# Optimization experiments

Measured on AMD Instinct MI355X. Metric: run time of the kernel, lower is better.

The kernel has to match this reference:

```python
import jax, jax.numpy as jnp
import numpy as np

B, S, D = 2, 4096, 2048
H = 16
HD = D // H          # head dim = 128
CHUNK = 64           # chunk size for O(N) chunked linear attention


def setup_inputs() -> dict:
    key = jax.random.key(0)
    ks = jax.random.split(key, 5)
    w = D ** -0.5  # fan-in init scale
    return {
        "x": jax.random.normal(ks[0], (B, S, D), jnp.float32),
        "Wq": jax.random.normal(ks[1], (D, D), jnp.float32) * w,
        "Wk": jax.random.normal(ks[2], (D, D), jnp.float32) * w,
        "Wv": jax.random.normal(ks[3], (D, D), jnp.float32) * w,
        "Wo": jax.random.normal(ks[4], (D, D), jnp.float32) * w,
    }


def _chunk_linear_attn(q, k, v):
    """Causal linear attention (identity feature map), chunked recurrent form.
    q, k, v: [b, h, n, d]. Equivalent to o_t = sum_{s<=t} (q_t . k_s) v_s.
    """
    b, h, n, d = q.shape
    nc = n // CHUNK
    q = q.reshape(b, h, nc, CHUNK, d)
    k = k.reshape(b, h, nc, CHUNK, d)
    v = v.reshape(b, h, nc, CHUNK, d)
    # intra-chunk causal part
    attn = jnp.einsum('bhncd,bhnsd->bhncs', q, k)
    causal = jnp.tril(jnp.ones((CHUNK, CHUNK), dtype=bool))
    attn = jnp.where(causal, attn, jnp.zeros((), attn.dtype))
    o_intra = jnp.einsum('bhncs,bhnsd->bhncd', attn, v)
    # inter-chunk recurrent state: S_i = sum_{j < i} K_j^T V_j  ([d, d] per head)
    kv = jnp.einsum('bhnsd,bhnse->bhnde', k, v)
    S = jnp.cumsum(kv, axis=2) - kv  # exclusive prefix sum over chunks
    o_inter = jnp.einsum('bhncd,bhnde->bhnce', q, S)
    return (o_intra + o_inter).reshape(b, h, n, d)


def reference(x, Wq, Wk, Wv, Wo):
    # bias-free projections (nn.Linear convention: y = x @ W.T)
    q = (x @ Wq.T).reshape(B, S, H, HD).transpose(0, 2, 1, 3)
    k = (x @ Wk.T).reshape(B, S, H, HD).transpose(0, 2, 1, 3)
    v = (x @ Wv.T).reshape(B, S, H, HD).transpose(0, 2, 1, 3)
    scale = HD ** -0.5  # fla chunk_linear_attn default scale on q
    o = _chunk_linear_attn(q * scale, k, v)
    o = o.transpose(0, 2, 1, 3).reshape(B, S, D)
    return o @ Wo.T
```

## Files before the change

### kernel.cpp

```cpp
#include <hip/hip_runtime.h>

typedef unsigned short u16;
typedef __attribute__((ext_vector_type(8))) short short8;
typedef __attribute__((ext_vector_type(8))) unsigned short u16x8;
typedef __attribute__((ext_vector_type(4))) unsigned short u16x4;
typedef __attribute__((ext_vector_type(2))) unsigned short u16x2;
typedef __attribute__((ext_vector_type(4))) float f32x4;

#define NBATCH 2
#define SEQ    4096
#define DIM    2048
#define NHEAD  16
#define HD     128
#define CH     64
#define NC     64
#define MROWS  8192

__device__ __forceinline__ float b2f(u16 u) {
    unsigned x = ((unsigned)u) << 16;
    return __builtin_bit_cast(float, x);
}
__device__ __forceinline__ u16 f2b(float f) {
    unsigned u = __builtin_bit_cast(unsigned, f);
    u += 0x7fffu + ((u >> 16) & 1u);
    return (u16)(u >> 16);
}

__device__ __forceinline__ void gload_lds16(const u16* g, u16* l) {
    __builtin_amdgcn_global_load_lds(
        (const __attribute__((address_space(1))) void*)g,
        (__attribute__((address_space(3))) void*)l, 16, 0, 0);
}

__global__ __launch_bounds__(256) void cast_all(
    const float* __restrict__ x,
    const float* __restrict__ w0, const float* __restrict__ w1,
    const float* __restrict__ w2, const float* __restrict__ w3,
    u16* __restrict__ xo,
    u16* __restrict__ o0, u16* __restrict__ o1,
    u16* __restrict__ o2, u16* __restrict__ o3)
{
    const int blk = blockIdx.x;
    const float* in;
    u16* out;
    long i;
    if (blk < 8192) {
        in = x; out = xo;
        i = (long)blk * 256 + threadIdx.x;
    } else {
        const int seg = (blk - 8192) >> 11;
        in  = seg == 0 ? w0 : seg == 1 ? w1 : seg == 2 ? w2 : w3;
        out = seg == 0 ? o0 : seg == 1 ? o1 : seg == 2 ? o2 : o3;
        i = (long)((blk - 8192) & 2047) * 256 + threadIdx.x;
    }
    f32x4 a = ((const f32x4*)in)[2 * i];
    f32x4 b = ((const f32x4*)in)[2 * i + 1];
    u16x8 o;
#pragma unroll
    for (int j = 0; j < 4; j++) { o[j] = f2b(a[j]); o[4 + j] = f2b(b[j]); }
    ((u16x8*)out)[i] = o;
}

#define GBM 256
#define GBN 256
#define GBK 32
#define BUFE 16384

struct Ctx8 {
    int wave, lane, wr, wc, m16, quad;
    int fl;
    long grA[2];
    int ldso[2];
};

__device__ __forceinline__ Ctx8 ctx8(int K) {
    Ctx8 c;
    const int tid = threadIdx.x;
    c.wave = tid >> 6; c.lane = tid & 63;
    c.wr = c.wave >> 2; c.wc = c.wave & 3;
    c.m16 = c.lane & 15; c.quad = (c.lane >> 4) & 3;
    const int t3 = c.lane >> 3;
    const int u3 = (c.lane & 7) ^ t3;
    const int ml = 2 * t3 + (u3 >> 2);
    const int sl = (u3 & 3) * 8;
#pragma unroll
    for (int i = 0; i < 2; i++) {
        const int bi = 2 * c.wave + i;
        c.grA[i] = (long)(bi * 16 + ml) * K + sl;
        c.ldso[i] = bi * 512 + c.lane * 8;
    }
    const int line = c.m16 >> 1;
    c.fl = line * 64 + ((((c.m16 & 1) << 2) | c.quad) ^ line) * 8;
    return c;
}

template<bool STG>
__device__ __forceinline__ void tile8(
    const Ctx8& c, const u16* As, const u16* Bs, f32x4 (&acc)[8][4],
    const u16* pA, const u16* pB, long ktN, u16* AsN, u16* BsN)
{
    short8 af[4], bf[4];
#pragma unroll
    for (int t = 0; t < 4; t++)
        af[t] = *(const short8*)&As[(c.wr * 8 + t) * 512 + c.fl];
#pragma unroll
    for (int t = 0; t < 4; t++)
        bf[t] = *(const short8*)&Bs[(c.wc * 4 + t) * 512 + c.fl];
    if (STG) {
        gload_lds16(pA + c.grA[0] + ktN, AsN + c.ldso[0]);
        gload_lds16(pA + c.grA[1] + ktN, AsN + c.ldso[1]);
    }
    __builtin_amdgcn_s_setprio(1);
#pragma unroll
    for (int i = 0; i < 4; i++)
#pragma unroll
        for (int j = 0; j < 4; j++)
            acc[i][j] = __builtin_amdgcn_mfma_f32_16x16x32_bf16(
                af[i], bf[j], acc[i][j], 0, 0, 0);
    __builtin_amdgcn_s_setprio(0);

#pragma unroll
    for (int t = 0; t < 4; t++)
        af[t] = *(const short8*)&As[(c.wr * 8 + 4 + t) * 512 + c.fl];
    if (STG) {
        gload_lds16(pB + c.grA[0] + ktN, BsN + c.ldso[0]);
        gload_lds16(pB + c.grA[1] + ktN, BsN + c.ldso[1]);
    }
    __builtin_amdgcn_s_setprio(1);
#pragma unroll
    for (int i = 0; i < 4; i++)
#pragma unroll
        for (int j = 0; j < 4; j++)
            acc[4 + i][j] = __builtin_amdgcn_mfma_f32_16x16x32_bf16(
                af[i], bf[j], acc[4 + i][j], 0, 0, 0);
    __builtin_amdgcn_s_setprio(0);
}

__device__ __forceinline__ void kloop8(
    const Ctx8& c, const u16* pA, const u16* pB, int K, u16* L, f32x4 (&acc)[8][4])
{
    const int NT = K >> 5;
#pragma unroll
    for (int t = 0; t < 3; t++) {
        u16* As = L + t * BUFE;
        u16* Bs = As + 8192;
        gload_lds16(pA + c.grA[0] + t * GBK, As + c.ldso[0]);
        gload_lds16(pA + c.grA[1] + t * GBK, As + c.ldso[1]);
        gload_lds16(pB + c.grA[0] + t * GBK, Bs + c.ldso[0]);
        gload_lds16(pB + c.grA[1] + t * GBK, Bs + c.ldso[1]);
    }
#pragma unroll 1
    for (int u = 0; u < NT - 3; ++u) {
        asm volatile("s_waitcnt vmcnt(8)" ::: "memory");
        __builtin_amdgcn_s_barrier();
        asm volatile("" ::: "memory");
        u16* As  = L + (u & 3) * BUFE;
        u16* AsN = L + ((u + 3) & 3) * BUFE;
        tile8<true>(c, As, As + 8192, acc, pA, pB, (long)(u + 3) * GBK,
                    AsN, AsN + 8192);
    }
    {
        const int u = NT - 3;
        asm volatile("s_waitcnt vmcnt(8)" ::: "memory");
        __builtin_amdgcn_s_barrier();
        asm volatile("" ::: "memory");
        u16* As = L + (u & 3) * BUFE;
        tile8<false>(c, As, As + 8192, acc, pA, pB, 0, nullptr, nullptr);
    }
    {
        const int u = NT - 2;
        asm volatile("s_waitcnt vmcnt(4)" ::: "memory");
        __builtin_amdgcn_s_barrier();
        asm volatile("" ::: "memory");
        u16* As = L + (u & 3) * BUFE;
        tile8<false>(c, As, As + 8192, acc, pA, pB, 0, nullptr, nullptr);
    }
    {
        const int u = NT - 1;
        asm volatile("s_waitcnt vmcnt(0)" ::: "memory");
        __builtin_amdgcn_s_barrier();
        asm volatile("" ::: "memory");
        u16* As = L + (u & 3) * BUFE;
        tile8<false>(c, As, As + 8192, acc, pA, pB, 0, nullptr, nullptr);
    }
}

__global__ __launch_bounds__(512, 2) void gemm_qkv(
    const u16* __restrict__ A,
    const u16* __restrict__ Wqb, const u16* __restrict__ Wkb, const u16* __restrict__ Wvb,
    u16* __restrict__ q, u16* __restrict__ k, u16* __restrict__ kt,
    u16* __restrict__ vt, float qscale)
{
    __shared__ __align__(16) u16 L[4 * BUFE];
    const Ctx8 c = ctx8(DIM);

    const int w = blockIdx.y >> 3;
    const long row0 = (long)blockIdx.x * GBM;
    const long col0 = (long)(blockIdx.y & 7) * GBN;
    const u16* Bw = w == 0 ? Wqb : w == 1 ? Wkb : Wvb;

    f32x4 acc[8][4];
#pragma unroll
    for (int i = 0; i < 8; i++)
#pragma unroll
        for (int j = 0; j < 4; j++) {
            f32x4 z = {0.f, 0.f, 0.f, 0.f};
            acc[i][j] = z;
        }

    kloop8(c, A + row0 * DIM, Bw + col0 * DIM, DIM, L, acc);

    const float scale = (w == 0) ? qscale : 1.0f;
#pragma unroll
    for (int i = 0; i < 8; i++) {
        const long grow0 = row0 + c.wr * 128 + i * 16 + c.quad * 4;
#pragma unroll
        for (int j = 0; j < 4; j++) {
            const long gcol = col0 + c.wc * 64 + j * 16 + c.m16;
            u16x4 p;
#pragma unroll
            for (int r = 0; r < 4; r++) p[r] = f2b(acc[i][j][r] * scale);
            if (w == 0) {
#pragma unroll
                for (int r = 0; r < 4; r++) q[(grow0 + r) * DIM + gcol] = p[r];
            } else {
                const long b = grow0 >> 12;
                const long t0 = grow0 & (SEQ - 1);
                u16* Ct = (w == 1) ? kt : vt;
                *(u16x4*)(Ct + (b * DIM + gcol) * SEQ + t0) = p;
                if (w == 1) {
#pragma unroll
                    for (int r = 0; r < 4; r++) k[(grow0 + r) * DIM + gcol] = p[r];
                }
            }
        }
    }
}

__global__ __launch_bounds__(512, 2) void gemm_out(
    const u16* __restrict__ A, const u16* __restrict__ Bw, float* __restrict__ C)
{
    __shared__ __align__(16) u16 L[4 * BUFE];
    const Ctx8 c = ctx8(DIM);
    const long row0 = (long)blockIdx.x * GBM;
    const long col0 = (long)blockIdx.y * GBN;

    f32x4 acc[8][4];
#pragma unroll
    for (int i = 0; i < 8; i++)
#pragma unroll
        for (int j = 0; j < 4; j++) {
            f32x4 z = {0.f, 0.f, 0.f, 0.f};
            acc[i][j] = z;
        }

    kloop8(c, A + row0 * DIM, Bw + col0 * DIM, DIM, L, acc);

#pragma unroll
    for (int i = 0; i < 8; i++) {
        const long grow0 = row0 + c.wr * 128 + i * 16 + c.quad * 4;
#pragma unroll
        for (int j = 0; j < 4; j++) {
            const long gcol = col0 + c.wc * 64 + j * 16 + c.m16;
#pragma unroll
            for (int r = 0; r < 4; r++)
                C[(grow0 + r) * DIM + gcol] = acc[i][j][r];
        }
    }
}

__global__ __launch_bounds__(256) void chunk_kv_mfma(
    const u16* __restrict__ Vt, const u16* __restrict__ Kt, u16* __restrict__ KV)
{
    const int tid = threadIdx.x, blk = blockIdx.x;
    const int c = blk & (NC - 1), bh = blk >> 6;
    const int wave = tid >> 6, lane = tid & 63;
    const int wr = wave >> 1, wc = wave & 1;
    const int m16 = lane & 15, quad = lane >> 4;
    const u16* vb = Vt + (long)bh * HD * SEQ + c * CH;
    const u16* kb = Kt + (long)bh * HD * SEQ + c * CH;

    f32x4 acc[4][4];
#pragma unroll
    for (int i = 0; i < 4; i++)
#pragma unroll
        for (int j = 0; j < 4; j++) {
            f32x4 z = {0.f, 0.f, 0.f, 0.f};
            acc[i][j] = z;
        }

#pragma unroll
    for (int tk = 0; tk < 2; tk++) {
        short8 af[4], bf[4];
#pragma unroll
        for (int t = 0; t < 4; t++)
            af[t] = *(const short8*)(vb + (long)(wr * 64 + t * 16 + m16) * SEQ + tk * 32 + quad * 8);
#pragma unroll
        for (int t = 0; t < 4; t++)
            bf[t] = *(const short8*)(kb + (long)(wc * 64 + t * 16 + m16) * SEQ + tk * 32 + quad * 8);
#pragma unroll
        for (int i = 0; i < 4; i++)
#pragma unroll
            for (int j = 0; j < 4; j++)
                acc[i][j] = __builtin_amdgcn_mfma_f32_16x16x32_bf16(
                    af[i], bf[j], acc[i][j], 0, 0, 0);
    }

    u16* outp = KV + (long)blk * (HD * HD);
#pragma unroll
    for (int i = 0; i < 4; i++)
#pragma unroll
        for (int j = 0; j < 4; j++)
#pragma unroll
            for (int r = 0; r < 4; r++)
                outp[(wr * 64 + i * 16 + quad * 4 + r) * HD + wc * 64 + j * 16 + m16]
                    = f2b(acc[i][j][r]);
}

__global__ __launch_bounds__(256) void kv_prefix(u16* __restrict__ KV)
{
    const int bh  = blockIdx.x >> 5;
    const int sub = blockIdx.x & 31;
    const long base = (long)bh * NC * (HD * HD) + (sub * 256 + threadIdx.x) * 2;
    float s0 = 0.f, s1 = 0.f;
#pragma unroll 4
    for (int c = 0; c < NC; c++) {
        u16* p = KV + base + (long)c * (HD * HD);
        u16x2 v = *(u16x2*)p;
        u16x2 w; w[0] = f2b(s0); w[1] = f2b(s1);
        *(u16x2*)p = w;
        s0 += b2f(v[0]); s1 += b2f(v[1]);
    }
}

#define AMP 72

__global__ __launch_bounds__(256) void chunk_out_mfma(
    const u16* __restrict__ Q, const u16* __restrict__ Kn,
    const u16* __restrict__ Vt, const u16* __restrict__ Sb, u16* __restrict__ O)
{
    __shared__ __align__(16) u16 Am[CH * AMP];

    const int tid = threadIdx.x, blk = blockIdx.x;
    const int c = blk & (NC - 1), bh = blk >> 6;
    const int h = bh & (NHEAD - 1), b = bh >> 4;
    const long rowbase = (long)b * SEQ + (long)c * CH;
    const int wave = tid >> 6, lane = tid & 63;
    const int m16 = lane & 15, quad = lane >> 4;

    const u16* qrow = Q  + (rowbase + wave * 16 + m16) * DIM + h * HD;
    const u16* krow = Kn + rowbase * DIM + h * HD;

    short8 qa[4];
#pragma unroll
    for (int dk = 0; dk < 4; dk++)
        qa[dk] = *(const short8*)(qrow + dk * 32 + quad * 8);

    f32x4 acc1[4];
#pragma unroll
    for (int jt = 0; jt < 4; jt++) {
        f32x4 z = {0.f, 0.f, 0.f, 0.f};
        acc1[jt] = z;
    }
#pragma unroll
    for (int dk = 0; dk < 4; dk++)
#pragma unroll
        for (int jt = 0; jt < 4; jt++) {
            short8 bb = *(const short8*)(krow + (long)(jt * 16 + m16) * DIM + dk * 32 + quad * 8);
            acc1[jt] = __builtin_amdgcn_mfma_f32_16x16x32_bf16(qa[dk], bb, acc1[jt], 0, 0, 0);
        }
    const int mbase = wave * 16 + quad * 4;
#pragma unroll
    for (int jt = 0; jt < 4; jt++) {
        const int j = jt * 16 + m16;
#pragma unroll
        for (int r = 0; r < 4; r++) {
            float v = (j <= mbase + r) ? acc1[jt][r] : 0.f;
            Am[(mbase + r) * AMP + j] = f2b(v);
        }
    }

    f32x4 acc[8];
#pragma unroll
    for (int et = 0; et < 8; et++) {
        f32x4 z = {0.f, 0.f, 0.f, 0.f};
        acc[et] = z;
    }
    const u16* Sg = Sb + (long)blk * (HD * HD);
#pragma unroll
    for (int dk = 0; dk < 4; dk++)
#pragma unroll
        for (int et = 0; et < 8; et++) {
            short8 sb = *(const short8*)(Sg + (et * 16 + m16) * HD + dk * 32 + quad * 8);
            acc[et] = __builtin_amdgcn_mfma_f32_16x16x32_bf16(qa[dk], sb, acc[et], 0, 0, 0);
        }

    __syncthreads();
    const u16* vb = Vt + (long)bh * HD * SEQ + c * CH;
#pragma unroll
    for (int tk = 0; tk < 2; tk++) {
        short8 a = *(const short8*)&Am[(wave * 16 + m16) * AMP + tk * 32 + quad * 8];
#pragma unroll
        for (int et = 0; et < 8; et++) {
            short8 vbf = *(const short8*)(vb + (long)(et * 16 + m16) * SEQ + tk * 32 + quad * 8);
            acc[et] = __builtin_amdgcn_mfma_f32_16x16x32_bf16(a, vbf, acc[et], 0, 0, 0);
        }
    }

#pragma unroll
    for (int et = 0; et < 8; et++) {
        const int e = et * 16 + m16;
#pragma unroll
        for (int r = 0; r < 4; r++) {
            const int m = wave * 16 + quad * 4 + r;
            O[(rowbase + m) * DIM + h * HD + e] = f2b(acc[et][r]);
        }
    }
}

extern "C" void kernel_launch(void* const* d_in, const int* in_sizes, int n_in,
                              void* d_out, int out_size, void* d_ws, size_t ws_size,
                              hipStream_t stream)
{
    (void)in_sizes; (void)n_in; (void)out_size; (void)ws_size;
    const float* x  = (const float*)d_in[0];
    const float* Wq = (const float*)d_in[1];
    const float* Wk = (const float*)d_in[2];
    const float* Wv = (const float*)d_in[3];
    const float* Wo = (const float*)d_in[4];
    float* out = (float*)d_out;

    const long NE = (long)MROWS * DIM;
    const long WE = (long)DIM * DIM;
    u16* xb  = (u16*)d_ws;
    u16* Wqb = xb  + NE;
    u16* Wkb = Wqb + WE;
    u16* Wvb = Wkb + WE;
    u16* Wob = Wvb + WE;
    u16* q   = Wob + WE;
    u16* k   = q + NE;
    u16* vt  = k + NE;
    u16* kv  = vt + NE;
    u16* o   = xb;
    u16* kt  = (u16*)d_out;

    hipLaunchKernelGGL(cast_all, dim3(16384), dim3(256), 0, stream,
                       x, Wq, Wk, Wv, Wo, xb, Wqb, Wkb, Wvb, Wob);

    const float qscale = 0.08838834764831845f;

    hipLaunchKernelGGL(gemm_qkv, dim3(MROWS / GBM, 24), dim3(512), 0, stream,
                       xb, Wqb, Wkb, Wvb, q, k, kt, vt, qscale);

    hipLaunchKernelGGL(chunk_kv_mfma, dim3(NBATCH * NHEAD * NC), dim3(256), 0, stream, vt, kt, kv);
    hipLaunchKernelGGL(kv_prefix,     dim3(1024),                dim3(256), 0, stream, kv);
    hipLaunchKernelGGL(chunk_out_mfma,dim3(NBATCH * NHEAD * NC), dim3(256), 0, stream, q, k, vt, kv, o);

    hipLaunchKernelGGL(gemm_out, dim3(MROWS / GBM, DIM / GBN), dim3(512), 0, stream, o, Wob, out);
}
```

Baseline: 553.5 us.

## Split GEMM k-step into barrier-synced phases and swizzle block order to XCDs

```diff
diff --git a/kernel.cpp b/kernel.cpp
--- a/kernel.cpp
+++ b/kernel.cpp
@@ -94,46 +94,39 @@
     return c;
 }
 
-template<bool STG>
-__device__ __forceinline__ void tile8(
-    const Ctx8& c, const u16* As, const u16* Bs, f32x4 (&acc)[8][4],
-    const u16* pA, const u16* pB, long ktN, u16* AsN, u16* BsN)
-{
-    short8 af[4], bf[4];
+template<bool READB, bool STG, int VMC>
+__device__ __forceinline__ void phase8(
+    const Ctx8& c, const u16* As, const u16* Bs, const int ihalf,
+    short8 (&bf)[4], f32x4 (&acc)[8][4],
+    const u16* pS, long off, u16* dst)
+{
+    short8 af[4];
 #pragma unroll
     for (int t = 0; t < 4; t++)
-        af[t] = *(const short8*)&As[(c.wr * 8 + t) * 512 + c.fl];
-#pragma unroll
-    for (int t = 0; t < 4; t++)
-        bf[t] = *(const short8*)&Bs[(c.wc * 4 + t) * 512 + c.fl];
+        af[t] = *(const short8*)&As[(c.wr * 8 + ihalf * 4 + t) * 512 + c.fl];
+    if (READB) {
+#pragma unroll
+        for (int t = 0; t < 4; t++)
+            bf[t] = *(const short8*)&Bs[(c.wc * 4 + t) * 512 + c.fl];
+    }
     if (STG) {
-        gload_lds16(pA + c.grA[0] + ktN, AsN + c.ldso[0]);
-        gload_lds16(pA + c.grA[1] + ktN, AsN + c.ldso[1]);
-    }
+        gload_lds16(pS + c.grA[0] + off, dst + c.ldso[0]);
+        gload_lds16(pS + c.grA[1] + off, dst + c.ldso[1]);
+    }
+    if (VMC >= 0)
+        asm volatile("s_waitcnt vmcnt(%0)" :: "i"(VMC < 0 ? 0 : VMC) : "memory");
+    __builtin_amdgcn_s_barrier();
+    asm volatile("s_waitcnt lgkmcnt(0)" ::: "memory");
+    __builtin_amdgcn_sched_barrier(0);
     __builtin_amdgcn_s_setprio(1);
 #pragma unroll
     for (int i = 0; i < 4; i++)
 #pragma unroll
         for (int j = 0; j < 4; j++)
-            acc[i][j] = __builtin_amdgcn_mfma_f32_16x16x32_bf16(
-                af[i], bf[j], acc[i][j], 0, 0, 0);
+            acc[ihalf * 4 + i][j] = __builtin_amdgcn_mfma_f32_16x16x32_bf16(
+                af[i], bf[j], acc[ihalf * 4 + i][j], 0, 0, 0);
     __builtin_amdgcn_s_setprio(0);
-
-#pragma unroll
-    for (int t = 0; t < 4; t++)
-        af[t] = *(const short8*)&As[(c.wr * 8 + 4 + t) * 512 + c.fl];
-    if (STG) {
-        gload_lds16(pB + c.grA[0] + ktN, BsN + c.ldso[0]);
-        gload_lds16(pB + c.grA[1] + ktN, BsN + c.ldso[1]);
-    }
-    __builtin_amdgcn_s_setprio(1);
-#pragma unroll
-    for (int i = 0; i < 4; i++)
-#pragma unroll
-        for (int j = 0; j < 4; j++)
-            acc[4 + i][j] = __builtin_amdgcn_mfma_f32_16x16x32_bf16(
-                af[i], bf[j], acc[4 + i][j], 0, 0, 0);
-    __builtin_amdgcn_s_setprio(0);
+    __builtin_amdgcn_s_barrier();
 }
 
 __device__ __forceinline__ void kloop8(
@@ -149,39 +142,33 @@
         gload_lds16(pB + c.grA[0] + t * GBK, Bs + c.ldso[0]);
         gload_lds16(pB + c.grA[1] + t * GBK, Bs + c.ldso[1]);
     }
+    asm volatile("s_waitcnt vmcnt(8)" ::: "memory");
+    __builtin_amdgcn_s_barrier();
+
+    short8 bf[4];
 #pragma unroll 1
     for (int u = 0; u < NT - 3; ++u) {
-        asm volatile("s_waitcnt vmcnt(8)" ::: "memory");
-        __builtin_amdgcn_s_barrier();
-        asm volatile("" ::: "memory");
-        u16* As  = L + (u & 3) * BUFE;
+        const u16* As = L + (u & 3) * BUFE;
+        const u16* Bs = As + 8192;
         u16* AsN = L + ((u + 3) & 3) * BUFE;
-        tile8<true>(c, As, As + 8192, acc, pA, pB, (long)(u + 3) * GBK,
-                    AsN, AsN + 8192);
+        const long off = (long)(u + 3) * GBK;
+        phase8<true,  true, -1>(c, As, Bs, 0, bf, acc, pA, off, AsN);
+        phase8<false, true,  8>(c, As, Bs, 1, bf, acc, pB, off, AsN + 8192);
     }
     {
-        const int u = NT - 3;
-        asm volatile("s_waitcnt vmcnt(8)" ::: "memory");
-        __builtin_amdgcn_s_barrier();
-        asm volatile("" ::: "memory");
-        u16* As = L + (u & 3) * BUFE;
-        tile8<false>(c, As, As + 8192, acc, pA, pB, 0, nullptr, nullptr);
+        const u16* As = L + ((NT - 3) & 3) * BUFE;
+        phase8<true,  false, -1>(c, As, As + 8192, 0, bf, acc, nullptr, 0, nullptr);
+        phase8<false, false,  4>(c, As, As + 8192, 1, bf, acc, nullptr, 0, nullptr);
     }
     {
-        const int u = NT - 2;
-        asm volatile("s_waitcnt vmcnt(4)" ::: "memory");
-        __builtin_amdgcn_s_barrier();
-        asm volatile("" ::: "memory");
-        u16* As = L + (u & 3) * BUFE;
-        tile8<false>(c, As, As + 8192, acc, pA, pB, 0, nullptr, nullptr);
+        const u16* As = L + ((NT - 2) & 3) * BUFE;
+        phase8<true,  false, -1>(c, As, As + 8192, 0, bf, acc, nullptr, 0, nullptr);
+        phase8<false, false,  0>(c, As, As + 8192, 1, bf, acc, nullptr, 0, nullptr);
     }
     {
-        const int u = NT - 1;
-        asm volatile("s_waitcnt vmcnt(0)" ::: "memory");
-        __builtin_amdgcn_s_barrier();
-        asm volatile("" ::: "memory");
-        u16* As = L + (u & 3) * BUFE;
-        tile8<false>(c, As, As + 8192, acc, pA, pB, 0, nullptr, nullptr);
+        const u16* As = L + ((NT - 1) & 3) * BUFE;
+        phase8<true,  false, -1>(c, As, As + 8192, 0, bf, acc, nullptr, 0, nullptr);
+        phase8<false, false, -1>(c, As, As + 8192, 1, bf, acc, nullptr, 0, nullptr);
     }
 }
 
@@ -194,9 +181,13 @@
     __shared__ __align__(16) u16 L[4 * BUFE];
     const Ctx8 c = ctx8(DIM);
 
-    const int w = blockIdx.y >> 3;
-    const long row0 = (long)blockIdx.x * GBM;
-    const long col0 = (long)(blockIdx.y & 7) * GBN;
+    const int lid = blockIdx.x;
+    const int swz = (lid & 7) * 96 + (lid >> 3);
+    const int bx = swz & 31;
+    const int by = swz >> 5;
+    const int w = by >> 3;
+    const long row0 = (long)bx * GBM;
+    const long col0 = (long)(by & 7) * GBN;
     const u16* Bw = w == 0 ? Wqb : w == 1 ? Wkb : Wvb;
 
     f32x4 acc[8][4];
@@ -242,8 +233,10 @@
 {
     __shared__ __align__(16) u16 L[4 * BUFE];
     const Ctx8 c = ctx8(DIM);
-    const long row0 = (long)blockIdx.x * GBM;
-    const long col0 = (long)blockIdx.y * GBN;
+    const int lid = blockIdx.x;
+    const int swz = (lid & 7) * 32 + (lid >> 3);
+    const long row0 = (long)(swz & 31) * GBM;
+    const long col0 = (long)(swz >> 5) * GBN;
 
     f32x4 acc[8][4];
 #pragma unroll
@@ -449,12 +442,12 @@
 
     const float qscale = 0.08838834764831845f;
 
-    hipLaunchKernelGGL(gemm_qkv, dim3(MROWS / GBM, 24), dim3(512), 0, stream,
+    hipLaunchKernelGGL(gemm_qkv, dim3(768), dim3(512), 0, stream,
                        xb, Wqb, Wkb, Wvb, q, k, kt, vt, qscale);
 
     hipLaunchKernelGGL(chunk_kv_mfma, dim3(NBATCH * NHEAD * NC), dim3(256), 0, stream, vt, kt, kv);
     hipLaunchKernelGGL(kv_prefix,     dim3(1024),                dim3(256), 0, stream, kv);
     hipLaunchKernelGGL(chunk_out_mfma,dim3(NBATCH * NHEAD * NC), dim3(256), 0, stream, q, k, vt, kv, o);
 
-    hipLaunchKernelGGL(gemm_out, dim3(MROWS / GBM, DIM / GBN), dim3(512), 0, stream, o, Wob, out);
-}
+    hipLaunchKernelGGL(gemm_out, dim3(256), dim3(512), 0, stream, o, Wob, out);
+}
```

Measured after the change: 599.2 us. +8.2%, slower.

## Software-pipeline LDS fragment loads across GEMM k-steps and widen prefix-scan vectors

Applied to the files above, without the earlier changes.

```diff
diff --git a/kernel.cpp b/kernel.cpp
--- a/kernel.cpp
+++ b/kernel.cpp
@@ -94,21 +94,26 @@
     return c;
 }
 
-template<bool STG>
-__device__ __forceinline__ void tile8(
-    const Ctx8& c, const u16* As, const u16* Bs, f32x4 (&acc)[8][4],
-    const u16* pA, const u16* pB, long ktN, u16* AsN, u16* BsN)
-{
-    short8 af[4], bf[4];
+template<bool STG, int VMC, bool PRE1>
+__device__ __forceinline__ void gstep(
+    const Ctx8& c, u16* L, int u,
+    short8 (&afC)[4], short8 (&afN)[4],
+    short8 (&bfC)[4], short8 (&bfN)[4],
+    f32x4 (&acc)[8][4],
+    const u16* pA, const u16* pB)
+{
+    const u16* S0 = L + (u & 3) * BUFE;
+    const u16* S1 = L + ((u + 1) & 3) * BUFE;
+    u16* SN = L + ((u + 3) & 3) * BUFE;
+    const long off = (long)(u + 3) * GBK;
+
+    __builtin_amdgcn_s_barrier();
 #pragma unroll
     for (int t = 0; t < 4; t++)
-        af[t] = *(const short8*)&As[(c.wr * 8 + t) * 512 + c.fl];
-#pragma unroll
-    for (int t = 0; t < 4; t++)
-        bf[t] = *(const short8*)&Bs[(c.wc * 4 + t) * 512 + c.fl];
+        afN[t] = *(const short8*)&S0[(c.wr * 8 + 4 + t) * 512 + c.fl];
     if (STG) {
-        gload_lds16(pA + c.grA[0] + ktN, AsN + c.ldso[0]);
-        gload_lds16(pA + c.grA[1] + ktN, AsN + c.ldso[1]);
+        gload_lds16(pA + c.grA[0] + off, SN + c.ldso[0]);
+        gload_lds16(pA + c.grA[1] + off, SN + c.ldso[1]);
     }
     __builtin_amdgcn_s_setprio(1);
 #pragma unroll
@@ -116,15 +121,23 @@
 #pragma unroll
         for (int j = 0; j < 4; j++)
             acc[i][j] = __builtin_amdgcn_mfma_f32_16x16x32_bf16(
-                af[i], bf[j], acc[i][j], 0, 0, 0);
+                afC[i], bfC[j], acc[i][j], 0, 0, 0);
     __builtin_amdgcn_s_setprio(0);
 
-#pragma unroll
-    for (int t = 0; t < 4; t++)
-        af[t] = *(const short8*)&As[(c.wr * 8 + 4 + t) * 512 + c.fl];
+    if (VMC >= 0)
+        asm volatile("s_waitcnt vmcnt(%0)" :: "i"(VMC < 0 ? 0 : VMC) : "memory");
+    __builtin_amdgcn_s_barrier();
+    if (PRE1) {
+#pragma unroll
+        for (int t = 0; t < 4; t++)
+            afC[t] = *(const short8*)&S1[(c.wr * 8 + t) * 512 + c.fl];
+#pragma unroll
+        for (int t = 0; t < 4; t++)
+            bfN[t] = *(const short8*)&S1[8192 + (c.wc * 4 + t) * 512 + c.fl];
+    }
     if (STG) {
-        gload_lds16(pB + c.grA[0] + ktN, BsN + c.ldso[0]);
-        gload_lds16(pB + c.grA[1] + ktN, BsN + c.ldso[1]);
+        gload_lds16(pB + c.grA[0] + off, SN + 8192 + c.ldso[0]);
+        gload_lds16(pB + c.grA[1] + off, SN + 8192 + c.ldso[1]);
     }
     __builtin_amdgcn_s_setprio(1);
 #pragma unroll
@@ -132,7 +145,7 @@
 #pragma unroll
         for (int j = 0; j < 4; j++)
             acc[4 + i][j] = __builtin_amdgcn_mfma_f32_16x16x32_bf16(
-                af[i], bf[j], acc[4 + i][j], 0, 0, 0);
+                afN[i], bfC[j], acc[4 + i][j], 0, 0, 0);
     __builtin_amdgcn_s_setprio(0);
 }
 
@@ -143,46 +156,30 @@
 #pragma unroll
     for (int t = 0; t < 3; t++) {
         u16* As = L + t * BUFE;
-        u16* Bs = As + 8192;
         gload_lds16(pA + c.grA[0] + t * GBK, As + c.ldso[0]);
         gload_lds16(pA + c.grA[1] + t * GBK, As + c.ldso[1]);
-        gload_lds16(pB + c.grA[0] + t * GBK, Bs + c.ldso[0]);
-        gload_lds16(pB + c.grA[1] + t * GBK, Bs + c.ldso[1]);
-    }
+        gload_lds16(pB + c.grA[0] + t * GBK, As + 8192 + c.ldso[0]);
+        gload_lds16(pB + c.grA[1] + t * GBK, As + 8192 + c.ldso[1]);
+    }
+    short8 afA[4], afB[4], bfA[4], bfB[4];
+    asm volatile("s_waitcnt vmcnt(8)" ::: "memory");
+    __builtin_amdgcn_s_barrier();
+#pragma unroll
+    for (int t = 0; t < 4; t++)
+        afA[t] = *(const short8*)&L[(c.wr * 8 + t) * 512 + c.fl];
+#pragma unroll
+    for (int t = 0; t < 4; t++)
+        bfA[t] = *(const short8*)&L[8192 + (c.wc * 4 + t) * 512 + c.fl];
+
 #pragma unroll 1
-    for (int u = 0; u < NT - 3; ++u) {
-        asm volatile("s_waitcnt vmcnt(8)" ::: "memory");
-        __builtin_amdgcn_s_barrier();
-        asm volatile("" ::: "memory");
-        u16* As  = L + (u & 3) * BUFE;
-        u16* AsN = L + ((u + 3) & 3) * BUFE;
-        tile8<true>(c, As, As + 8192, acc, pA, pB, (long)(u + 3) * GBK,
-                    AsN, AsN + 8192);
-    }
-    {
-        const int u = NT - 3;
-        asm volatile("s_waitcnt vmcnt(8)" ::: "memory");
-        __builtin_amdgcn_s_barrier();
-        asm volatile("" ::: "memory");
-        u16* As = L + (u & 3) * BUFE;
-        tile8<false>(c, As, As + 8192, acc, pA, pB, 0, nullptr, nullptr);
-    }
-    {
-        const int u = NT - 2;
-        asm volatile("s_waitcnt vmcnt(4)" ::: "memory");
-        __builtin_amdgcn_s_barrier();
-        asm volatile("" ::: "memory");
-        u16* As = L + (u & 3) * BUFE;
-        tile8<false>(c, As, As + 8192, acc, pA, pB, 0, nullptr, nullptr);
-    }
-    {
-        const int u = NT - 1;
-        asm volatile("s_waitcnt vmcnt(0)" ::: "memory");
-        __builtin_amdgcn_s_barrier();
-        asm volatile("" ::: "memory");
-        u16* As = L + (u & 3) * BUFE;
-        tile8<false>(c, As, As + 8192, acc, pA, pB, 0, nullptr, nullptr);
-    }
+    for (int u = 0; u < NT - 4; u += 2) {
+        gstep<true, 6, true>(c, L, u,     afA, afB, bfA, bfB, acc, pA, pB);
+        gstep<true, 6, true>(c, L, u + 1, afA, afB, bfB, bfA, acc, pA, pB);
+    }
+    gstep<true,  6, true >(c, L, NT - 4, afA, afB, bfA, bfB, acc, pA, pB);
+    gstep<false, 4, true >(c, L, NT - 3, afA, afB, bfB, bfA, acc, pA, pB);
+    gstep<false, 0, true >(c, L, NT - 2, afA, afB, bfA, bfB, acc, pA, pB);
+    gstep<false, -1, false>(c, L, NT - 1, afA, afB, bfB, bfA, acc, pA, pB);
 }
 
 __global__ __launch_bounds__(512, 2) void gemm_qkv(
@@ -319,17 +316,18 @@
 
 __global__ __launch_bounds__(256) void kv_prefix(u16* __restrict__ KV)
 {
-    const int bh  = blockIdx.x >> 5;
-    const int sub = blockIdx.x & 31;
-    const long base = (long)bh * NC * (HD * HD) + (sub * 256 + threadIdx.x) * 2;
-    float s0 = 0.f, s1 = 0.f;
+    const int bh  = blockIdx.x >> 4;
+    const int sub = blockIdx.x & 15;
+    const long base = (long)bh * NC * (HD * HD) + (sub * 256 + threadIdx.x) * 4;
+    float s0 = 0.f, s1 = 0.f, s2 = 0.f, s3 = 0.f;
 #pragma unroll 4
     for (int c = 0; c < NC; c++) {
         u16* p = KV + base + (long)c * (HD * HD);
-        u16x2 v = *(u16x2*)p;
-        u16x2 w; w[0] = f2b(s0); w[1] = f2b(s1);
-        *(u16x2*)p = w;
-        s0 += b2f(v[0]); s1 += b2f(v[1]);
+        u16x4 v = *(u16x4*)p;
+        u16x4 w;
+        w[0] = f2b(s0); w[1] = f2b(s1); w[2] = f2b(s2); w[3] = f2b(s3);
+        *(u16x4*)p = w;
+        s0 += b2f(v[0]); s1 += b2f(v[1]); s2 += b2f(v[2]); s3 += b2f(v[3]);
     }
 }
 
@@ -453,7 +451,7 @@
                        xb, Wqb, Wkb, Wvb, q, k, kt, vt, qscale);
 
     hipLaunchKernelGGL(chunk_kv_mfma, dim3(NBATCH * NHEAD * NC), dim3(256), 0, stream, vt, kt, kv);
-    hipLaunchKernelGGL(kv_prefix,     dim3(1024),                dim3(256), 0, stream, kv);
+    hipLaunchKernelGGL(kv_prefix,     dim3(512),                 dim3(256), 0, stream, kv);
     hipLaunchKernelGGL(chunk_out_mfma,dim3(NBATCH * NHEAD * NC), dim3(256), 0, stream, q, k, vt, kv, o);
 
     hipLaunchKernelGGL(gemm_out, dim3(MROWS / GBM, DIM / GBN), dim3(512), 0, stream, o, Wob, out);
```

After: 532.6 us. 1.04x faster.
